# Kernel tuning notes

Hardware: AMD Instinct MI355X
Metric: run time of the kernel (lower is better)

Reference implementation:

```python
import jax, jax.numpy as jnp
import numpy as np

NUM_PTS = 1024
LATENT_SIZE = 32
BETA = 0.1


def setup_inputs() -> dict:
    key = jax.random.key(0)
    k1, k2, k3, k4 = jax.random.split(key, 4)
    B = 128
    return {
        "recon_x": jax.random.normal(k1, (B, NUM_PTS, 3), dtype=jnp.float32),
        "x": jax.random.normal(k2, (B, NUM_PTS, 3), dtype=jnp.float32),
        "mu": jax.random.normal(k3, (B, LATENT_SIZE), dtype=jnp.float32),
        "logvar": jax.random.normal(k4, (B, LATENT_SIZE), dtype=jnp.float32),
    }


def _chamfer(recon_x, x):
    # Batched squared pairwise distances: P[b, i, j] = ||x[b,i] - recon_x[b,j]||^2
    xx = jnp.sum(x * x, axis=-1)              # [B, N]
    yy = jnp.sum(recon_x * recon_x, axis=-1)  # [B, N]
    xy = jnp.einsum("bnd,bmd->bnm", x, recon_x)  # [B, N, N]
    P = xx[:, :, None] + yy[:, None, :] - 2.0 * xy
    # Bidirectional min + sum
    loss_1 = jnp.sum(jnp.min(P, axis=1))  # for each recon point, nearest x point
    loss_2 = jnp.sum(jnp.min(P, axis=2))  # for each x point, nearest recon point
    return loss_1 + loss_2


def reference(recon_x, x, mu, logvar):
    RE = _chamfer(recon_x, x) / NUM_PTS
    KLD = -0.5 * jnp.sum(1.0 + logvar - mu * mu - jnp.exp(logvar))
    KLD = KLD / LATENT_SIZE
    return RE + KLD * BETA
```

## Files before the change

kernel.cpp:

```cpp
#include <hip/hip_runtime.h>

#define NUM_PTS 1024
#define NBATCH 128
#define BT 1024
#define NW 16
#define QW 64
#define R 8
#define NSTEP 64
#define RING_PAD 132
#define CHAMF_SCALE (1.0f / 1024.0f)
#define KLD_SCALE   (-0.5f * 0.1f / 32.0f)

#define COL_OFF 0
#define RS_OFF  (256 * 1024)
#define WS2_OFF (RS_OFF + 256)

__global__ __launch_bounds__(BT, 4) void chamfer_shared(
    const float* __restrict__ recon_x,
    const float* __restrict__ x,
    float* __restrict__ ws)
{
    const int bid = blockIdx.x;
    const int b   = bid >> 1;
    const int rh  = bid & 1;
    const int w   = threadIdx.x >> 6;
    const int lt  = threadIdx.x & 63;
    const int t   = threadIdx.x;

    __shared__ float4 ring[NW][RING_PAD];
    __shared__ float  red[NW];

    {
        const float* qsrc = recon_x + (size_t)b * NUM_PTS * 3 + (size_t)(w * QW + lt) * 3;
        const float qx = qsrc[0], qy = qsrc[1], qz = qsrc[2];
        const float4 q4 = make_float4(qx, qy, qz,
                                      fmaf(qx, qx, fmaf(qy, qy, qz * qz)));
        ring[w][lt]      = q4;
        ring[w][lt + 64] = q4;
    }

    const float* rp = x + (size_t)b * NUM_PTS * 3 + (size_t)rh * 512 * 3;
    float vx[R], vy[R], vz[R], r2[R], m[R];
    {
        float buf[24];
        const float4* __restrict__ s4 = (const float4*)(rp + 24 * lt);
        float4* bp = (float4*)buf;
#pragma unroll
        for (int i = 0; i < 6; ++i) bp[i] = s4[i];
#pragma unroll
        for (int k = 0; k < R; ++k) {
            vx[k] = -2.0f * buf[3 * k + 0];
            vy[k] = -2.0f * buf[3 * k + 1];
            vz[k] = -2.0f * buf[3 * k + 2];
            r2[k] = 0.25f * fmaf(vx[k], vx[k], fmaf(vy[k], vy[k], vz[k] * vz[k]));
            m[k]  = 1e30f;
        }
    }

    const float4* __restrict__ ringw = &ring[w][lt];
    float ca = 1e30f;
    const int rotaddr = ((lt + 1) & 63) << 2;
    float4 qA = ringw[0];
    float4 qB = ringw[1];

#pragma unroll 4
    for (int s = 0; s < NSTEP; s += 2) {
        const float4 qC = ringw[s + 2];
        const float4 qD = ringw[s + 3];
        float da[R], db[R];
#pragma unroll
        for (int r = 0; r < R; ++r)
            da[r] = fmaf(vx[r], qA.x, fmaf(vy[r], qA.y, fmaf(vz[r], qA.z, r2[r] + qA.w)));
        {
            const float t0 = fminf(fminf(da[0], da[1]), da[2]);
            const float t1 = fminf(fminf(da[3], da[4]), da[5]);
            const float t2 = fminf(fminf(da[6], da[7]), ca);
            ca = fminf(fminf(t0, t1), t2);
        }
        ca = __int_as_float(__builtin_amdgcn_ds_bpermute(rotaddr, __float_as_int(ca)));
#pragma unroll
        for (int r = 0; r < R; ++r)
            db[r] = fmaf(vx[r], qB.x, fmaf(vy[r], qB.y, fmaf(vz[r], qB.z, r2[r] + qB.w)));
#pragma unroll
        for (int r = 0; r < R; ++r)
            m[r] = fminf(fminf(m[r], da[r]), db[r]);
        {
            const float u0 = fminf(fminf(db[0], db[1]), db[2]);
            const float u1 = fminf(fminf(db[3], db[4]), db[5]);
            const float u2 = fminf(fminf(db[6], db[7]), ca);
            ca = fminf(fminf(u0, u1), u2);
        }
        ca = __int_as_float(__builtin_amdgcn_ds_bpermute(rotaddr, __float_as_int(ca)));
        qA = qC;
        qB = qD;
    }

    ws[COL_OFF + (size_t)bid * 1024 + w * QW + lt] = ca;

    {
        float* mrow = (float*)&ring[w][0];
#pragma unroll
        for (int k = 0; k < R; ++k)
            mrow[R * lt + k] = m[k];
    }
    __syncthreads();

    float v = 0.0f;
    if (t < 512) {
        const float* cb = (const float*)&ring[0][0];
        v = cb[t];
#pragma unroll
        for (int ww = 1; ww < NW; ++ww)
            v = fminf(v, cb[ww * (RING_PAD * 4) + t]);
        for (int off = 32; off > 0; off >>= 1)
            v += __shfl_down(v, off, 64);
        if (lt == 0) red[w] = v;
    }
    __syncthreads();
    if (t == 0) {
        float s = 0.f;
#pragma unroll
        for (int ww = 0; ww < 8; ++ww) s += red[ww];
        ws[RS_OFF + bid] = s;
    }
}

__global__ __launch_bounds__(256) void colfold(float* __restrict__ ws)
{
    const int b = blockIdx.x;
    const int t = threadIdx.x;
    const float4* p0 = (const float4*)(ws + COL_OFF + (size_t)(2 * b)     * 1024) + t;
    const float4* p1 = (const float4*)(ws + COL_OFF + (size_t)(2 * b + 1) * 1024) + t;
    const float4 a = *p0;
    const float4 c = *p1;
    float v = fminf(a.x, c.x) + fminf(a.y, c.y) + fminf(a.z, c.z) + fminf(a.w, c.w);
    for (int off = 32; off > 0; off >>= 1)
        v += __shfl_down(v, off, 64);
    __shared__ float red[4];
    if ((t & 63) == 0) red[t >> 6] = v;
    __syncthreads();
    if (t == 0) {
        float s = red[0] + red[1] + red[2] + red[3];
        s += ws[RS_OFF + 2 * b] + ws[RS_OFF + 2 * b + 1];
        ws[WS2_OFF + b] = s;
    }
}

__global__ __launch_bounds__(128) void final_k(
    const float* __restrict__ ws,
    const float* __restrict__ mu,
    const float* __restrict__ logvar,
    float* __restrict__ out)
{
    const int t = threadIdx.x;
    float v = ws[WS2_OFF + t] * CHAMF_SCALE;

    const float4* mp = (const float4*)mu + 8 * t;
    const float4* lp = (const float4*)logvar + 8 * t;
    float kv = 0.f;
#pragma unroll
    for (int i = 0; i < 8; ++i) {
        const float4 mm = mp[i];
        const float4 lv = lp[i];
        kv += (1.f + lv.x - mm.x * mm.x - expf(lv.x));
        kv += (1.f + lv.y - mm.y * mm.y - expf(lv.y));
        kv += (1.f + lv.z - mm.z * mm.z - expf(lv.z));
        kv += (1.f + lv.w - mm.w * mm.w - expf(lv.w));
    }
    v += kv * KLD_SCALE;

    for (int off = 32; off > 0; off >>= 1)
        v += __shfl_down(v, off, 64);
    __shared__ float red[2];
    if ((t & 63) == 0) red[t >> 6] = v;
    __syncthreads();
    if (t == 0) out[0] = red[0] + red[1];
}

extern "C" void kernel_launch(void* const* d_in, const int* in_sizes, int n_in,
                              void* d_out, int out_size, void* d_ws, size_t ws_size,
                              hipStream_t stream) {
    const float* recon_x = (const float*)d_in[0];
    const float* x       = (const float*)d_in[1];
    const float* mu      = (const float*)d_in[2];
    const float* logvar  = (const float*)d_in[3];
    float* out = (float*)d_out;
    float* ws  = (float*)d_ws;

    chamfer_shared<<<2 * NBATCH, BT, 0, stream>>>(recon_x, x, ws);
    colfold<<<NBATCH, 256, 0, stream>>>(ws);
    final_k<<<1, 128, 0, stream>>>(ws, mu, logvar, out);
}
```

Baseline: 77.80 us.

## Use DPP row rotation for column-min passing and fuse final reduction via atomics

Replaces the per-step ds_bpermute lane rotation of the running column minimum with a cheaper DPP row_ror within 16-lane rows. The shared ring is re-laid out into four 16-entry groups, and only one cross-row bpermute is done per phase. A runtime probe checks the DPP rotation direction to pick the right access order. The separate final kernel is removed: the KLD term is folded into colfold and per-batch sums go to the output via atomicAdd. This saves a launch but makes the float summation order nondeterministic.

```diff
diff --git a/kernel.cpp b/kernel.cpp
--- a/kernel.cpp
+++ b/kernel.cpp
@@ -4,21 +4,74 @@
 #define NBATCH 128
 #define BT 1024
 #define NW 16
-#define QW 64
 #define R 8
-#define NSTEP 64
-#define RING_PAD 132
 #define CHAMF_SCALE (1.0f / 1024.0f)
 #define KLD_SCALE   (-0.5f * 0.1f / 32.0f)
 
 #define COL_OFF 0
 #define RS_OFF  (256 * 1024)
-#define WS2_OFF (RS_OFF + 256)
+
+#define ROW_ROR1 0x121
+
+__device__ __forceinline__ float rotr1(float v) {
+    return __int_as_float(__builtin_amdgcn_update_dpp(
+        0, __float_as_int(v), ROW_ROR1, 0xF, 0xF, true));
+}
+
+template <int DIR>
+__device__ __forceinline__ float rot_phases(
+    const float4* __restrict__ ringw, int k, int g, int xaddr,
+    const float* vx, const float* vy, const float* vz, const float* r2,
+    float* m)
+{
+    float ca = 1e30f;
+#pragma unroll 1
+    for (int p = 0; p < 4; ++p) {
+        const int W = (g + p) & 3;
+        const float4* __restrict__ rw = ringw + (W * 32 + k);
+#pragma unroll
+        for (int sp = 0; sp < 8; ++sp) {
+            const int s0 = 2 * sp;
+            const int s1 = s0 + 1;
+            const int o0 = (DIR == 0) ? s0 : ((16 - s0) & 15);
+            const int o1 = (DIR == 0) ? s1 : ((16 - s1) & 15);
+            const float4 qa = rw[o0];
+            const float4 qb = rw[o1];
+            float da[R], db[R];
+#pragma unroll
+            for (int r = 0; r < R; ++r)
+                da[r] = fmaf(vx[r], qa.x, fmaf(vy[r], qa.y, fmaf(vz[r], qa.z, r2[r] + qa.w)));
+            {
+                const float t0 = fminf(fminf(da[0], da[1]), da[2]);
+                const float t1 = fminf(fminf(da[3], da[4]), da[5]);
+                const float t2 = fminf(fminf(da[6], da[7]), ca);
+                ca = fminf(fminf(t0, t1), t2);
+            }
+            ca = rotr1(ca);
+#pragma unroll
+            for (int r = 0; r < R; ++r)
+                db[r] = fmaf(vx[r], qb.x, fmaf(vy[r], qb.y, fmaf(vz[r], qb.z, r2[r] + qb.w)));
+#pragma unroll
+            for (int r = 0; r < R; ++r)
+                m[r] = fminf(fminf(m[r], da[r]), db[r]);
+            {
+                const float u0 = fminf(fminf(db[0], db[1]), db[2]);
+                const float u1 = fminf(fminf(db[3], db[4]), db[5]);
+                const float u2 = fminf(fminf(db[6], db[7]), ca);
+                ca = fminf(fminf(u0, u1), u2);
+            }
+            ca = rotr1(ca);
+        }
+        ca = __int_as_float(__builtin_amdgcn_ds_bpermute(xaddr, __float_as_int(ca)));
+    }
+    return ca;
+}
 
 __global__ __launch_bounds__(BT, 4) void chamfer_shared(
     const float* __restrict__ recon_x,
     const float* __restrict__ x,
-    float* __restrict__ ws)
+    float* __restrict__ ws,
+    float* __restrict__ out)
 {
     const int bid = blockIdx.x;
     const int b   = bid >> 1;
@@ -27,16 +80,19 @@
     const int lt  = threadIdx.x & 63;
     const int t   = threadIdx.x;
 
-    __shared__ float4 ring[NW][RING_PAD];
+    if (bid == 0 && t == 0) out[0] = 0.0f;
+
+    __shared__ float4 ring2[NW][128];
     __shared__ float  red[NW];
 
     {
-        const float* qsrc = recon_x + (size_t)b * NUM_PTS * 3 + (size_t)(w * QW + lt) * 3;
+        const float* qsrc = recon_x + (size_t)b * NUM_PTS * 3 + (size_t)(w * 64 + lt) * 3;
         const float qx = qsrc[0], qy = qsrc[1], qz = qsrc[2];
         const float4 q4 = make_float4(qx, qy, qz,
                                       fmaf(qx, qx, fmaf(qy, qy, qz * qz)));
-        ring[w][lt]      = q4;
-        ring[w][lt + 64] = q4;
+        const int Wl = lt >> 4, jl = lt & 15;
+        ring2[w][Wl * 32 + jl]      = q4;
+        ring2[w][Wl * 32 + 16 + jl] = q4;
     }
 
     const float* rp = x + (size_t)b * NUM_PTS * 3 + (size_t)rh * 512 * 3;
@@ -57,61 +113,32 @@
         }
     }
 
-    const float4* __restrict__ ringw = &ring[w][lt];
-    float ca = 1e30f;
-    const int rotaddr = ((lt + 1) & 63) << 2;
-    float4 qA = ringw[0];
-    float4 qB = ringw[1];
+    const int k = lt & 15, g = lt >> 4;
+    const int xaddr = ((lt + 16) & 63) << 2;
+    const int probe = __builtin_amdgcn_update_dpp(0, lt, ROW_ROR1, 0xF, 0xF, true);
+    float ca;
+    if (probe == ((lt & 48) | ((lt + 1) & 15)))
+        ca = rot_phases<0>(&ring2[w][0], k, g, xaddr, vx, vy, vz, r2, m);
+    else
+        ca = rot_phases<1>(&ring2[w][0], k, g, xaddr, vx, vy, vz, r2, m);
 
-#pragma unroll 4
-    for (int s = 0; s < NSTEP; s += 2) {
-        const float4 qC = ringw[s + 2];
-        const float4 qD = ringw[s + 3];
-        float da[R], db[R];
-#pragma unroll
-        for (int r = 0; r < R; ++r)
-            da[r] = fmaf(vx[r], qA.x, fmaf(vy[r], qA.y, fmaf(vz[r], qA.z, r2[r] + qA.w)));
-        {
-            const float t0 = fminf(fminf(da[0], da[1]), da[2]);
-            const float t1 = fminf(fminf(da[3], da[4]), da[5]);
-            const float t2 = fminf(fminf(da[6], da[7]), ca);
-            ca = fminf(fminf(t0, t1), t2);
-        }
-        ca = __int_as_float(__builtin_amdgcn_ds_bpermute(rotaddr, __float_as_int(ca)));
-#pragma unroll
-        for (int r = 0; r < R; ++r)
-            db[r] = fmaf(vx[r], qB.x, fmaf(vy[r], qB.y, fmaf(vz[r], qB.z, r2[r] + qB.w)));
-#pragma unroll
-        for (int r = 0; r < R; ++r)
-            m[r] = fminf(fminf(m[r], da[r]), db[r]);
-        {
-            const float u0 = fminf(fminf(db[0], db[1]), db[2]);
-            const float u1 = fminf(fminf(db[3], db[4]), db[5]);
-            const float u2 = fminf(fminf(db[6], db[7]), ca);
-            ca = fminf(fminf(u0, u1), u2);
-        }
-        ca = __int_as_float(__builtin_amdgcn_ds_bpermute(rotaddr, __float_as_int(ca)));
-        qA = qC;
-        qB = qD;
-    }
-
-    ws[COL_OFF + (size_t)bid * 1024 + w * QW + lt] = ca;
+    ws[COL_OFF + (size_t)bid * 1024 + w * 64 + lt] = ca;
 
     {
-        float* mrow = (float*)&ring[w][0];
+        float* mrow = (float*)&ring2[w][0];
 #pragma unroll
-        for (int k = 0; k < R; ++k)
-            mrow[R * lt + k] = m[k];
+        for (int kk = 0; kk < R; ++kk)
+            mrow[R * lt + kk] = m[kk];
     }
     __syncthreads();
 
     float v = 0.0f;
     if (t < 512) {
-        const float* cb = (const float*)&ring[0][0];
+        const float* cb = (const float*)&ring2[0][0];
         v = cb[t];
 #pragma unroll
         for (int ww = 1; ww < NW; ++ww)
-            v = fminf(v, cb[ww * (RING_PAD * 4) + t]);
+            v = fminf(v, cb[ww * 512 + t]);
         for (int off = 32; off > 0; off >>= 1)
             v += __shfl_down(v, off, 64);
         if (lt == 0) red[w] = v;
@@ -125,7 +152,11 @@
     }
 }
 
-__global__ __launch_bounds__(256) void colfold(float* __restrict__ ws)
+__global__ __launch_bounds__(256) void colfold2(
+    const float* __restrict__ ws,
+    const float* __restrict__ mu,
+    const float* __restrict__ logvar,
+    float* __restrict__ out)
 {
     const int b = blockIdx.x;
     const int t = threadIdx.x;
@@ -133,7 +164,14 @@
     const float4* p1 = (const float4*)(ws + COL_OFF + (size_t)(2 * b + 1) * 1024) + t;
     const float4 a = *p0;
     const float4 c = *p1;
-    float v = fminf(a.x, c.x) + fminf(a.y, c.y) + fminf(a.z, c.z) + fminf(a.w, c.w);
+    float v = (fminf(a.x, c.x) + fminf(a.y, c.y)
+             + fminf(a.z, c.z) + fminf(a.w, c.w)) * CHAMF_SCALE;
+    if (t < 32) {
+        const int idx = b * 32 + t;
+        const float lv = logvar[idx];
+        const float mm = mu[idx];
+        v += (1.0f + lv - mm * mm - expf(lv)) * KLD_SCALE;
+    }
     for (int off = 32; off > 0; off >>= 1)
         v += __shfl_down(v, off, 64);
     __shared__ float red[4];
@@ -141,40 +179,9 @@
     __syncthreads();
     if (t == 0) {
         float s = red[0] + red[1] + red[2] + red[3];
-        s += ws[RS_OFF + 2 * b] + ws[RS_OFF + 2 * b + 1];
-        ws[WS2_OFF + b] = s;
+        s += (ws[RS_OFF + 2 * b] + ws[RS_OFF + 2 * b + 1]) * CHAMF_SCALE;
+        atomicAdd(out, s);
     }
-}
-
-__global__ __launch_bounds__(128) void final_k(
-    const float* __restrict__ ws,
-    const float* __restrict__ mu,
-    const float* __restrict__ logvar,
-    float* __restrict__ out)
-{
-    const int t = threadIdx.x;
-    float v = ws[WS2_OFF + t] * CHAMF_SCALE;
-
-    const float4* mp = (const float4*)mu + 8 * t;
-    const float4* lp = (const float4*)logvar + 8 * t;
-    float kv = 0.f;
-#pragma unroll
-    for (int i = 0; i < 8; ++i) {
-        const float4 mm = mp[i];
-        const float4 lv = lp[i];
-        kv += (1.f + lv.x - mm.x * mm.x - expf(lv.x));
-        kv += (1.f + lv.y - mm.y * mm.y - expf(lv.y));
-        kv += (1.f + lv.z - mm.z * mm.z - expf(lv.z));
-        kv += (1.f + lv.w - mm.w * mm.w - expf(lv.w));
-    }
-    v += kv * KLD_SCALE;
-
-    for (int off = 32; off > 0; off >>= 1)
-        v += __shfl_down(v, off, 64);
-    __shared__ float red[2];
-    if ((t & 63) == 0) red[t >> 6] = v;
-    __syncthreads();
-    if (t == 0) out[0] = red[0] + red[1];
 }
 
 extern "C" void kernel_launch(void* const* d_in, const int* in_sizes, int n_in,
@@ -187,7 +194,6 @@
     float* out = (float*)d_out;
     float* ws  = (float*)d_ws;
 
-    chamfer_shared<<<2 * NBATCH, BT, 0, stream>>>(recon_x, x, ws);
-    colfold<<<NBATCH, 256, 0, stream>>>(ws);
-    final_k<<<1, 128, 0, stream>>>(ws, mu, logvar, out);
+    chamfer_shared<<<2 * NBATCH, BT, 0, stream>>>(recon_x, x, ws, out);
+    colfold2<<<NBATCH, 256, 0, stream>>>(ws, mu, logvar, out);
 }
```

After: 79.56 us. +2.3%, slower.
